# Performance work log

Measured on AMD Instinct MI355X. Metric: run time of the kernel, lower is better.

## Reference

```python
import jax, jax.numpy as jnp
import numpy as np
import math

D_MODEL = 512
DIM_K = 512
DIM_V = 512
N_HEADS = 8


def setup_inputs() -> dict:
    key = jax.random.key(0)
    ks = jax.random.split(key, 12)
    B, S = 2, 2048
    sc = 1.0 / math.sqrt(D_MODEL)
    return {
        "x": jax.random.normal(ks[0], (B, S, D_MODEL), dtype=jnp.float32),
        "y": jax.random.normal(ks[1], (B, S, D_MODEL), dtype=jnp.float32),
        # weights stored [in, out] so linear is x @ W + b
        "Wq": jax.random.normal(ks[2], (D_MODEL, DIM_K), dtype=jnp.float32) * sc,
        "bq": jnp.zeros((DIM_K,), dtype=jnp.float32),
        "Wk": jax.random.normal(ks[3], (D_MODEL, DIM_K), dtype=jnp.float32) * sc,
        "bk": jnp.zeros((DIM_K,), dtype=jnp.float32),
        "Wv": jax.random.normal(ks[4], (D_MODEL, DIM_V), dtype=jnp.float32) * sc,
        "bv": jnp.zeros((DIM_V,), dtype=jnp.float32),
        "Wo": jax.random.normal(ks[5], (DIM_V, D_MODEL), dtype=jnp.float32) * sc,
        "bo": jnp.zeros((D_MODEL,), dtype=jnp.float32),
    }


def reference(x, y, Wq, bq, Wk, bk, Wv, bv, Wo, bo):
    B, S, _ = x.shape
    H = N_HEADS
    Dh = DIM_K // H
    Dvh = DIM_V // H
    norm = 1.0 / math.sqrt(D_MODEL)  # note: original scales by 1/sqrt(d_model)

    # torch: q(x).reshape(-1, B, S, Dh) -> heads on leading dim (row-major)
    Q = (x @ Wq + bq).reshape(-1, B, S, Dh)      # [H,B,S,Dh]
    K = (y @ Wk + bk).reshape(-1, B, S, Dh)      # [H,B,S,Dh]
    V = (y @ Wv + bv).reshape(-1, B, S, Dvh)     # [H,B,S,Dvh]

    scores = jnp.einsum('hbqd,hbkd->hbqk', Q, K) * norm  # [H,B,S,S]

    # median-threshold mask: torch.median on even n returns lower middle value
    med_idx = (S - 1) // 2
    thre = jnp.sort(scores, axis=-1)[..., med_idx:med_idx + 1]  # [H,B,S,1]
    masked = scores - thre <= 0  # mask where score <= median
    scores = jnp.where(masked, -jnp.inf, scores)

    attn = jax.nn.softmax(scores, axis=-1)
    # dropout omitted (deterministic / eval mode)
    out = jnp.einsum('hbqk,hbkd->hbqd', attn, V)  # [H,B,S,Dvh]
    out = out.reshape(B, S, -1)                   # faithful row-major reshape
    return out @ Wo + bo
```

## Files before the change

### kernel.cpp

```cpp
#include <hip/hip_runtime.h>
#include <hip/hip_bf16.h>
#include <stdint.h>

#define SEQ    2048
#define DMODEL 512
#define NPANEL 16
#define NORM   0.044194173824159216f

typedef _Float16 f16;
typedef __attribute__((ext_vector_type(8))) _Float16 half8;
typedef __attribute__((ext_vector_type(2))) _Float16 half2v;
typedef __attribute__((ext_vector_type(4))) float f32x4;
typedef __attribute__((ext_vector_type(4))) unsigned int u32x4;

__device__ __forceinline__ unsigned umin2(unsigned a, unsigned b){ return a<b?a:b; }
__device__ __forceinline__ unsigned umax2(unsigned a, unsigned b){ return a>b?a:b; }

__global__ __launch_bounds__(256) void k_cvt(const float4* __restrict__ x,
                                             const float4* __restrict__ y,
                                             f16* __restrict__ xh, f16* __restrict__ xl,
                                             f16* __restrict__ yh, f16* __restrict__ yl){
  int i = blockIdx.x*256 + threadIdx.x;
  float4 a = x[i]; float4 b = y[i];
  half2v h0 = {(f16)a.x, (f16)a.y}, h1 = {(f16)a.z, (f16)a.w};
  *(half2v*)(xh + i*4)     = h0; *(half2v*)(xh + i*4 + 2) = h1;
  half2v l0 = {(f16)(a.x-(float)h0[0]), (f16)(a.y-(float)h0[1])};
  half2v l1 = {(f16)(a.z-(float)h1[0]), (f16)(a.w-(float)h1[1])};
  *(half2v*)(xl + i*4)     = l0; *(half2v*)(xl + i*4 + 2) = l1;
  half2v g0 = {(f16)b.x, (f16)b.y}, g1 = {(f16)b.z, (f16)b.w};
  *(half2v*)(yh + i*4)     = g0; *(half2v*)(yh + i*4 + 2) = g1;
  half2v m0 = {(f16)(b.x-(float)g0[0]), (f16)(b.y-(float)g0[1])};
  half2v m1 = {(f16)(b.z-(float)g1[0]), (f16)(b.w-(float)g1[1])};
  *(half2v*)(yl + i*4)     = m0; *(half2v*)(yl + i*4 + 2) = m1;
}

__global__ __launch_bounds__(256) void k_wt(const float* __restrict__ Wq, const float* __restrict__ Wk,
                                            const float* __restrict__ Wv, const float* __restrict__ Wo,
                                            f16* __restrict__ Wth, f16* __restrict__ Wtl){
  int z = blockIdx.z;
  const float* W = (z==0)?Wq:(z==1)?Wk:(z==2)?Wv:Wo;
  __shared__ float tile[64][65];
  int k0 = blockIdx.x*64, n0 = blockIdx.y*64;
  #pragma unroll
  for (int i = 0; i < 16; ++i){
    int s = threadIdx.x + i*256; int kl2 = s>>6, nl = s&63;
    tile[kl2][nl] = W[(k0+kl2)*512 + (n0+nl)];
  }
  __syncthreads();
  #pragma unroll
  for (int i = 0; i < 16; ++i){
    int s = threadIdx.x + i*256; int nl = s>>6, kl2 = s&63;
    float v = tile[kl2][nl];
    f16 h = (f16)v;
    int idx = z*262144 + (n0+nl)*512 + (k0+kl2);
    Wth[idx] = h;
    Wtl[idx] = (f16)(v - (float)h);
  }
}

template<int FINAL>
__global__ __launch_bounds__(256) void k_gemm(const f16* __restrict__ Ah0, const f16* __restrict__ Al0,
                                              const f16* __restrict__ Ah1, const f16* __restrict__ Al1,
                                              const f16* __restrict__ Wh, const f16* __restrict__ Wl,
                                              const float* __restrict__ b0, const float* __restrict__ b1,
                                              const float* __restrict__ b2,
                                              f16* __restrict__ Oq, float* __restrict__ Of){
  int z = blockIdx.z;
  const f16* A  = (z==0) ? Ah0 : Ah1;
  const f16* Alp= (z==0) ? Al0 : Al1;
  const f16* Bh = Wh + z*262144;
  const f16* Bl = Wl + z*262144;
  const float* bias = (z==0)?b0:(z==1)?b1:b2;
  const bool split = (FINAL==0) && (z<2);
  int m0 = blockIdx.x*128, n0 = blockIdx.y*128;

  __shared__ f16 Ahs[128][40], Bhs[128][40], Als[128][40], Bls[128][40];

  int t = threadIdx.x, l = t&63, w = t>>6;
  int wr = w>>1, wc = w&1;
  int lr = l&15, lk = l>>4;

  f32x4 acc[4][4];
  #pragma unroll
  for (int i=0;i<4;++i)
    #pragma unroll
    for (int j=0;j<4;++j) acc[i][j] = (f32x4){0.f,0.f,0.f,0.f};

  for (int ks = 0; ks < 16; ++ks){
    int k0 = ks*32;
    #pragma unroll
    for (int i = 0; i < 2; ++i){
      int s = t + i*256; int r = s>>2, kc = s&3;
      *(u32x4*)(&Ahs[r][kc*8]) = *(const u32x4*)(A   + (m0+r)*512 + k0 + kc*8);
      *(u32x4*)(&Bhs[r][kc*8]) = *(const u32x4*)(Bh  + (n0+r)*512 + k0 + kc*8);
      if (split){
        *(u32x4*)(&Als[r][kc*8]) = *(const u32x4*)(Alp + (m0+r)*512 + k0 + kc*8);
        *(u32x4*)(&Bls[r][kc*8]) = *(const u32x4*)(Bl  + (n0+r)*512 + k0 + kc*8);
      }
    }
    __syncthreads();
    half8 ah[4], bh2[4], al2[4], bl2[4];
    #pragma unroll
    for (int tm = 0; tm < 4; ++tm) ah[tm]  = *(const half8*)(&Ahs[wr*64 + tm*16 + lr][lk*8]);
    #pragma unroll
    for (int tn = 0; tn < 4; ++tn) bh2[tn] = *(const half8*)(&Bhs[wc*64 + tn*16 + lr][lk*8]);
    if (split){
      #pragma unroll
      for (int tm = 0; tm < 4; ++tm) al2[tm] = *(const half8*)(&Als[wr*64 + tm*16 + lr][lk*8]);
      #pragma unroll
      for (int tn = 0; tn < 4; ++tn) bl2[tn] = *(const half8*)(&Bls[wc*64 + tn*16 + lr][lk*8]);
    }
    #pragma unroll
    for (int tm = 0; tm < 4; ++tm)
      #pragma unroll
      for (int tn = 0; tn < 4; ++tn){
        acc[tm][tn] = __builtin_amdgcn_mfma_f32_16x16x32_f16(ah[tm], bh2[tn], acc[tm][tn], 0,0,0);
        if (split){
          acc[tm][tn] = __builtin_amdgcn_mfma_f32_16x16x32_f16(ah[tm], bl2[tn], acc[tm][tn], 0,0,0);
          acc[tm][tn] = __builtin_amdgcn_mfma_f32_16x16x32_f16(al2[tm], bh2[tn], acc[tm][tn], 0,0,0);
        }
      }
    __syncthreads();
  }

  #pragma unroll
  for (int tn = 0; tn < 4; ++tn){
    int n_g = n0 + wc*64 + tn*16 + lr;
    float bv = bias[n_g];
    #pragma unroll
    for (int tm = 0; tm < 4; ++tm){
      #pragma unroll
      for (int r = 0; r < 4; ++r){
        int m_g = m0 + wr*64 + tm*16 + lk*4 + r;
        float v = acc[tm][tn][r] + bv;
        size_t idx = (size_t)m_g*512 + n_g;
        if (FINAL){
          Of[idx] = v;
        } else if (z < 2){
          f16 h = (f16)v;
          Oq[(size_t)z*4194304 + idx] = h;
          Oq[(size_t)z*4194304 + 2097152 + idx] = (f16)(v - (float)h);
        } else {
          Oq[(size_t)4*2097152 + idx] = (f16)v;
        }
      }
    }
  }
}

__global__ __launch_bounds__(256) void k_vt(const unsigned short* __restrict__ V, unsigned short* __restrict__ Vt){
  int p = blockIdx.y;
  int t = threadIdx.x;
  int d = t & 63, sc = t >> 6;
  int s0b = blockIdx.x*32 + sc*8;
  const unsigned short* Vp = V + p*131072;
  unsigned short* Vtp = Vt + p*131072;
  typedef __attribute__((ext_vector_type(8))) short short8;
  short8 vv;
  #pragma unroll
  for (int j = 0; j < 8; ++j) vv[j] = (short)Vp[(s0b + j)*64 + d];
  *(short8*)(Vtp + d*2048 + s0b) = vv;
}

__global__ __launch_bounds__(512, 4) void k_attn(const f16* __restrict__ Qh, const f16* __restrict__ Ql,
                                                 const f16* __restrict__ Kh, const f16* __restrict__ Kl,
                                                 const f16* __restrict__ Vt, f16* __restrict__ O){
  extern __shared__ char scb[];
  __shared__ float rzs[16];
  __shared__ float red[1024];
  int p = blockIdx.x, qt = blockIdx.y;
  int s0 = qt*16;
  const f16* Qhp = Qh + p*131072;
  const f16* Qlp = Ql + p*131072;
  const f16* Khp = Kh + p*131072;
  const f16* Klp = Kl + p*131072;
  const f16* Vtp = Vt + p*131072;
  int t = threadIdx.x, l = t&63, w = t>>6;
  int lr = l&15, lk = l>>4;

  half8 qh[2], ql[2];
  #pragma unroll
  for (int f = 0; f < 2; ++f){
    qh[f] = *(const half8*)(Qhp + (s0+lr)*64 + f*32 + lk*8);
    ql[f] = *(const half8*)(Qlp + (s0+lr)*64 + f*32 + lk*8);
  }

  {
    const f16* Kbase = Khp + (w*128 + lr)*64 + lk*8;
    const f16* Lbase = Klp + (w*128 + lr)*64 + lk*8;
    #pragma unroll
    for (int bt = 0; bt < 2; ++bt){
      half8 kb0[4], kb1[4], lb0[4], lb1[4];
      #pragma unroll
      for (int i = 0; i < 4; ++i){
        const f16* ka = Kbase + (bt*4 + i)*1024;
        const f16* la = Lbase + (bt*4 + i)*1024;
        kb0[i] = *(const half8*)(ka);
        kb1[i] = *(const half8*)(ka + 32);
        lb0[i] = *(const half8*)(la);
        lb1[i] = *(const half8*)(la + 32);
      }
      #pragma unroll
      for (int i = 0; i < 4; ++i){
        f32x4 c1 = (f32x4){0.f,0.f,0.f,0.f};
        f32x4 c2 = (f32x4){0.f,0.f,0.f,0.f};
        f32x4 c3 = (f32x4){0.f,0.f,0.f,0.f};
        c1 = __builtin_amdgcn_mfma_f32_16x16x32_f16(qh[0], kb0[i], c1, 0,0,0);
        c2 = __builtin_amdgcn_mfma_f32_16x16x32_f16(qh[0], lb0[i], c2, 0,0,0);
        c3 = __builtin_amdgcn_mfma_f32_16x16x32_f16(ql[0], kb0[i], c3, 0,0,0);
        c1 = __builtin_amdgcn_mfma_f32_16x16x32_f16(qh[1], kb1[i], c1, 0,0,0);
        c2 = __builtin_amdgcn_mfma_f32_16x16x32_f16(qh[1], lb1[i], c2, 0,0,0);
        c3 = __builtin_amdgcn_mfma_f32_16x16x32_f16(ql[1], kb1[i], c3, 0,0,0);
        int n = w*128 + (bt*4 + i)*16 + lr;
        #pragma unroll
        for (int r = 0; r < 4; ++r){
          int row = lk*4 + r;
          *(float*)(scb + row*4096 + (((unsigned)(n*4)) ^ ((unsigned)(lk<<6)))) = c1[r] + c2[r] + c3[r];
        }
      }
    }
  }
  __syncthreads();

  unsigned ovA0[16], ovA1[16];
  {
    int row0 = w*2;
    unsigned C = ((unsigned)((row0>>2)&3))<<6;
    const char* rb0 = scb + row0*4096;
    const char* rb1 = rb0 + 4096;
    #pragma unroll
    for (int j = 0; j < 16; ++j){
      unsigned off = (((unsigned)((l + j*64)*4)) ^ C);
      unsigned u0 = *(const unsigned*)(rb0 + off);
      unsigned u1 = *(const unsigned*)(rb1 + off);
      ovA0[j] = ((int)u0 < 0) ? ~u0 : (u0 | 0x80000000u);
      ovA1[j] = ((int)u1 < 0) ? ~u1 : (u1 | 0x80000000u);
    }
  }
  __syncthreads();

  {
    const f16* Kbase = Khp + (1024 + w*128 + lr)*64 + lk*8;
    const f16* Lbase = Klp + (1024 + w*128 + lr)*64 + lk*8;
    #pragma unroll
    for (int bt = 0; bt < 4; ++bt){
      half8 kb0[2], kb1[2], lb0[2], lb1[2];
      #pragma unroll
      for (int i = 0; i < 2; ++i){
        const f16* ka = Kbase + (bt*2 + i)*1024;
        const f16* la = Lbase + (bt*2 + i)*1024;
        kb0[i] = *(const half8*)(ka);
        kb1[i] = *(const half8*)(ka + 32);
        lb0[i] = *(const half8*)(la);
        lb1[i] = *(const half8*)(la + 32);
      }
      #pragma unroll
      for (int i = 0; i < 2; ++i){
        f32x4 c1 = (f32x4){0.f,0.f,0.f,0.f};
        f32x4 c2 = (f32x4){0.f,0.f,0.f,0.f};
        f32x4 c3 = (f32x4){0.f,0.f,0.f,0.f};
        c1 = __builtin_amdgcn_mfma_f32_16x16x32_f16(qh[0], kb0[i], c1, 0,0,0);
        c2 = __builtin_amdgcn_mfma_f32_16x16x32_f16(qh[0], lb0[i], c2, 0,0,0);
        c3 = __builtin_amdgcn_mfma_f32_16x16x32_f16(ql[0], kb0[i], c3, 0,0,0);
        c1 = __builtin_amdgcn_mfma_f32_16x16x32_f16(qh[1], kb1[i], c1, 0,0,0);
        c2 = __builtin_amdgcn_mfma_f32_16x16x32_f16(qh[1], lb1[i], c2, 0,0,0);
        c3 = __builtin_amdgcn_mfma_f32_16x16x32_f16(ql[1], kb1[i], c3, 0,0,0);
        int n = w*128 + (bt*2 + i)*16 + lr;
        #pragma unroll
        for (int r = 0; r < 4; ++r){
          int row = lk*4 + r;
          *(float*)(scb + row*4096 + (((unsigned)(n*4)) ^ ((unsigned)(lk<<6)))) = c1[r] + c2[r] + c3[r];
        }
      }
    }
  }
  __syncthreads();

  #pragma unroll 1
  for (int rr = 0; rr < 2; ++rr){
    int row = w*2 + rr;
    const char* rb = scb + row*4096;
    unsigned C = ((unsigned)((row>>2)&3))<<6;
    unsigned o2[16];
    #pragma unroll
    for (int j = 0; j < 16; ++j){
      unsigned u = *(const unsigned*)(rb + (((unsigned)((l + j*64)*4)) ^ C));
      o2[j] = ((int)u < 0) ? ~u : (u | 0x80000000u);
    }
    unsigned umn = 0xFFFFFFFFu, umx = 0u;
    #pragma unroll
    for (int j = 0; j < 16; ++j){
      unsigned a = (rr==0) ? ovA0[j] : ovA1[j];
      umn = umin2(umn, umin2(a, o2[j]));
      umx = umax2(umax2(umx, a), o2[j]);
    }
    #pragma unroll
    for (int off2 = 1; off2 < 64; off2 <<= 1){
      umn = umin2(umn, (unsigned)__shfl_xor((int)umn, off2));
      umx = umax2(umx, (unsigned)__shfl_xor((int)umx, off2));
    }
    unsigned thr;
    {
      unsigned L = umn, R = umx;
      #pragma unroll 1
      for (;;){
        if (L >= R){ thr = R; break; }
        unsigned mid = L + ((R - L) >> 1);
        int c = 0;
        #pragma unroll
        for (int j = 0; j < 16; ++j){
          unsigned a = (rr==0) ? ovA0[j] : ovA1[j];
          c += (int)__popcll(__ballot(a <= mid));
          c += (int)__popcll(__ballot(o2[j] <= mid));
        }
        if (c == 1024){ thr = mid; break; }
        if (c > 1024) R = mid; else L = mid + 1;
      }
    }
    unsigned bmx = (umx & 0x80000000u) ? (umx & 0x7FFFFFFFu) : ~umx;
    float mx = __uint_as_float(bmx);
    float zs = 0.f;
    unsigned g = ((unsigned)(row & 7)) << 4;
    char* pb = scb + row*4096;
    #pragma unroll
    for (int j = 0; j < 32; ++j){
      unsigned a = (j < 16) ? ((rr==0) ? ovA0[j] : ovA1[j]) : o2[j-16];
      unsigned b = (a & 0x80000000u) ? (a & 0x7FFFFFFFu) : ~a;
      float v = __uint_as_float(b);
      float wgt = (a <= thr) ? 0.f : __expf((v - mx) * NORM);
      zs += wgt;
      unsigned col = (unsigned)((j & 15)*64 + l + (j >> 4)*1024);
      *(f16*)(pb + ((col*2) ^ g)) = (f16)wgt;
    }
    #pragma unroll
    for (int off2 = 1; off2 < 64; off2 <<= 1) zs += __shfl_xor(zs, off2);
    if (l == 0) rzs[row] = 1.f / zs;
  }
  __syncthreads();

  int oc = w & 3, kh2 = w >> 2;
  const f16* vbase = Vtp + (oc*16 + lr)*2048 + kh2*1024 + lk*8;
  const char* pbase = scb + lr*4096;
  unsigned pswz = ((unsigned)(lr & 7)) << 4;
  f32x4 o0 = (f32x4){0.f,0.f,0.f,0.f};
  f32x4 o1 = (f32x4){0.f,0.f,0.f,0.f};
  #pragma unroll
  for (int kb2 = 0; kb2 < 8; ++kb2){
    half8 pa[4], vb[4];
    #pragma unroll
    for (int i = 0; i < 4; ++i){
      int kc = kb2*4 + i;
      pa[i] = *(const half8*)(pbase + (((unsigned)((kh2*1024 + kc*32 + lk*8)*2)) ^ pswz));
      vb[i] = *(const half8*)(vbase + kc*32);
    }
    o0 = __builtin_amdgcn_mfma_f32_16x16x32_f16(pa[0], vb[0], o0, 0,0,0);
    o1 = __builtin_amdgcn_mfma_f32_16x16x32_f16(pa[1], vb[1], o1, 0,0,0);
    o0 = __builtin_amdgcn_mfma_f32_16x16x32_f16(pa[2], vb[2], o0, 0,0,0);
    o1 = __builtin_amdgcn_mfma_f32_16x16x32_f16(pa[3], vb[3], o1, 0,0,0);
  }
  f32x4 oa;
  #pragma unroll
  for (int r = 0; r < 4; ++r) oa[r] = o0[r] + o1[r];
  if (kh2 == 1){
    #pragma unroll
    for (int r = 0; r < 4; ++r) red[oc*256 + (lk*4+r)*16 + lr] = oa[r];
  }
  __syncthreads();
  if (kh2 == 0){
    #pragma unroll
    for (int r = 0; r < 4; ++r){
      int row = lk*4 + r;
      float v = (oa[r] + red[oc*256 + row*16 + lr]) * rzs[row];
      O[p*131072 + (s0+row)*64 + oc*16 + lr] = (f16)v;
    }
  }
}

extern "C" void kernel_launch(void* const* d_in, const int* in_sizes, int n_in,
                              void* d_out, int out_size, void* d_ws, size_t ws_size,
                              hipStream_t stream) {
  const float* x  = (const float*)d_in[0];
  const float* y  = (const float*)d_in[1];
  const float* Wq = (const float*)d_in[2];
  const float* bq = (const float*)d_in[3];
  const float* Wk = (const float*)d_in[4];
  const float* bk = (const float*)d_in[5];
  const float* Wv = (const float*)d_in[6];
  const float* bv = (const float*)d_in[7];
  const float* Wo = (const float*)d_in[8];
  const float* bo = (const float*)d_in[9];

  f16* ws = (f16*)d_ws;
  f16* xh  = ws;
  f16* xl  = ws + 2097152;
  f16* yh  = ws + 4194304;
  f16* yl  = ws + 6291456;
  f16* Wth = ws + 8388608;
  f16* Wtl = ws + 9437184;
  f16* QKV = ws + 10485760;
  f16* Vt  = ws;
  f16* Ob  = ws + 2097152;

  (void)hipFuncSetAttribute(reinterpret_cast<const void*>(k_attn),
                            hipFuncAttributeMaxDynamicSharedMemorySize, 65536);

  k_cvt<<<2048, 256, 0, stream>>>((const float4*)x, (const float4*)y, xh, xl, yh, yl);
  k_wt<<<dim3(8,8,4), 256, 0, stream>>>(Wq, Wk, Wv, Wo, Wth, Wtl);
  k_gemm<0><<<dim3(32,4,3), 256, 0, stream>>>(xh, xl, yh, yl, Wth, Wtl, bq, bk, bv, QKV, nullptr);
  k_vt<<<dim3(64,16), 256, 0, stream>>>((const unsigned short*)(QKV + 4*2097152), (unsigned short*)Vt);
  k_attn<<<dim3(16,128), 512, 65536, stream>>>(QKV, QKV + 2097152, QKV + 2*2097152, QKV + 3*2097152, Vt, Ob);
  k_gemm<1><<<dim3(32,4,1), 256, 0, stream>>>(Ob, Ob, Ob, Ob, Wth + 3*262144, Wtl, bo, bo, bo, nullptr, (float*)d_out);
}
```

Measured before the change: 290.6 us.

## Speed up median selection with interpolation search and DPP wave reductions

Rewrites the per-row median threshold search. It starts from the row mean as the first pivot and alternates interpolation steps (using the counts at the bracket ends) with bisection steps, so fewer counting iterations should be needed. Counting now sums per-lane comparisons followed by a single DPP/readlane wave sum, instead of one ballot and popcount per element. The min, max and exp-sum reductions also switch from shfl_xor to DPP row shifts plus readlane. This adds a float division per step and extra control flow, and the quality of the interpolation depends on how the scores are distributed.

Measured after the change: 302.2 us. +4.0%, slower.

```diff
diff --git a/kernel.cpp b/kernel.cpp
--- a/kernel.cpp
+++ b/kernel.cpp
@@ -15,6 +15,116 @@
 
 __device__ __forceinline__ unsigned umin2(unsigned a, unsigned b){ return a<b?a:b; }
 __device__ __forceinline__ unsigned umax2(unsigned a, unsigned b){ return a>b?a:b; }
+
+__device__ __forceinline__ int wsum_i(int v){
+  v += __builtin_amdgcn_update_dpp(0, v, 0x111, 0xf, 0xf, true);
+  v += __builtin_amdgcn_update_dpp(0, v, 0x112, 0xf, 0xf, true);
+  v += __builtin_amdgcn_update_dpp(0, v, 0x114, 0xf, 0xf, true);
+  v += __builtin_amdgcn_update_dpp(0, v, 0x118, 0xf, 0xf, true);
+  return __builtin_amdgcn_readlane(v,15) + __builtin_amdgcn_readlane(v,31)
+       + __builtin_amdgcn_readlane(v,47) + __builtin_amdgcn_readlane(v,63);
+}
+__device__ __forceinline__ float wsum_f(float v){
+  float t;
+  t = __int_as_float(__builtin_amdgcn_update_dpp(0, __float_as_int(v), 0x111, 0xf, 0xf, true)); v += t;
+  t = __int_as_float(__builtin_amdgcn_update_dpp(0, __float_as_int(v), 0x112, 0xf, 0xf, true)); v += t;
+  t = __int_as_float(__builtin_amdgcn_update_dpp(0, __float_as_int(v), 0x114, 0xf, 0xf, true)); v += t;
+  t = __int_as_float(__builtin_amdgcn_update_dpp(0, __float_as_int(v), 0x118, 0xf, 0xf, true)); v += t;
+  float r = __int_as_float(__builtin_amdgcn_readlane(__float_as_int(v),15));
+  r += __int_as_float(__builtin_amdgcn_readlane(__float_as_int(v),31));
+  r += __int_as_float(__builtin_amdgcn_readlane(__float_as_int(v),47));
+  r += __int_as_float(__builtin_amdgcn_readlane(__float_as_int(v),63));
+  return r;
+}
+__device__ __forceinline__ unsigned wmin_u(unsigned v){
+  unsigned t;
+  t = (unsigned)__builtin_amdgcn_update_dpp((int)v,(int)v,0x111,0xf,0xf,false); v = umin2(v,t);
+  t = (unsigned)__builtin_amdgcn_update_dpp((int)v,(int)v,0x112,0xf,0xf,false); v = umin2(v,t);
+  t = (unsigned)__builtin_amdgcn_update_dpp((int)v,(int)v,0x114,0xf,0xf,false); v = umin2(v,t);
+  t = (unsigned)__builtin_amdgcn_update_dpp((int)v,(int)v,0x118,0xf,0xf,false); v = umin2(v,t);
+  return umin2(umin2((unsigned)__builtin_amdgcn_readlane((int)v,15),(unsigned)__builtin_amdgcn_readlane((int)v,31)),
+               umin2((unsigned)__builtin_amdgcn_readlane((int)v,47),(unsigned)__builtin_amdgcn_readlane((int)v,63)));
+}
+__device__ __forceinline__ unsigned wmax_u(unsigned v){
+  unsigned t;
+  t = (unsigned)__builtin_amdgcn_update_dpp((int)v,(int)v,0x111,0xf,0xf,false); v = umax2(v,t);
+  t = (unsigned)__builtin_amdgcn_update_dpp((int)v,(int)v,0x112,0xf,0xf,false); v = umax2(v,t);
+  t = (unsigned)__builtin_amdgcn_update_dpp((int)v,(int)v,0x114,0xf,0xf,false); v = umax2(v,t);
+  t = (unsigned)__builtin_amdgcn_update_dpp((int)v,(int)v,0x118,0xf,0xf,false); v = umax2(v,t);
+  return umax2(umax2((unsigned)__builtin_amdgcn_readlane((int)v,15),(unsigned)__builtin_amdgcn_readlane((int)v,31)),
+               umax2((unsigned)__builtin_amdgcn_readlane((int)v,47),(unsigned)__builtin_amdgcn_readlane((int)v,63)));
+}
+
+__device__ __forceinline__ void sel_row(const unsigned (&a)[16], const unsigned (&b)[16],
+                                        char* pb, float* rzs, int row, int l){
+  unsigned vmn = 0xFFFFFFFFu, vmx = 0u;
+  float fs = 0.f;
+  #pragma unroll
+  for (int j = 0; j < 16; ++j){
+    vmn = umin2(vmn, umin2(a[j], b[j]));
+    vmx = umax2(umax2(vmx, a[j]), b[j]);
+    unsigned ba = (a[j] & 0x80000000u) ? (a[j] & 0x7FFFFFFFu) : ~a[j];
+    unsigned bb = (b[j] & 0x80000000u) ? (b[j] & 0x7FFFFFFFu) : ~b[j];
+    fs += __uint_as_float(ba) + __uint_as_float(bb);
+  }
+  unsigned umn = wmin_u(vmn);
+  unsigned umx = wmax_u(vmx);
+  float mu = wsum_f(fs) * (1.0f/2048.0f);
+  unsigned bmu = __float_as_uint(mu);
+  unsigned emu = ((int)bmu < 0) ? ~bmu : (bmu | 0x80000000u);
+
+  unsigned thr;
+  {
+    unsigned L = umn, R = umx, cL = 0, cR = 2048, mid = emu;
+    int it = 0;
+    #pragma unroll 1
+    for (;;){
+      if (L >= R){ thr = R; break; }
+      if (mid < L) mid = L;
+      if (mid > R - 1) mid = R - 1;
+      int c0=0,c1=0,c2=0,c3=0;
+      #pragma unroll
+      for (int j = 0; j < 4; ++j){
+        c0 += (a[j]    <= mid); c1 += (a[j+4]  <= mid);
+        c2 += (a[j+8]  <= mid); c3 += (a[j+12] <= mid);
+        c0 += (b[j]    <= mid); c1 += (b[j+4]  <= mid);
+        c2 += (b[j+8]  <= mid); c3 += (b[j+12] <= mid);
+      }
+      int c = wsum_i((c0+c1)+(c2+c3));
+      if (c == 1024){ thr = mid; break; }
+      if (c > 1024){ R = mid; cR = (unsigned)c; }
+      else         { L = mid + 1; cL = (unsigned)c; }
+      if (L >= R){ thr = R; break; }
+      unsigned span = R - L;
+      unsigned off;
+      if (it & 1) off = span >> 1;
+      else {
+        float f = (float)(1024 - (int)cL) * (float)span / (float)((int)cR - (int)cL);
+        off = (unsigned)(int)f;
+      }
+      if (off >= span) off = span - 1;
+      mid = L + off;
+      ++it;
+    }
+  }
+
+  unsigned bmx = (umx & 0x80000000u) ? (umx & 0x7FFFFFFFu) : ~umx;
+  float mx = __uint_as_float(bmx);
+  float zs = 0.f;
+  unsigned g = ((unsigned)(row & 7)) << 4;
+  #pragma unroll
+  for (int j = 0; j < 32; ++j){
+    unsigned vv = (j < 16) ? a[j] : b[j-16];
+    unsigned bb = (vv & 0x80000000u) ? (vv & 0x7FFFFFFFu) : ~vv;
+    float v = __uint_as_float(bb);
+    float wgt = (vv <= thr) ? 0.f : __expf((v - mx) * NORM);
+    zs += wgt;
+    unsigned col = (unsigned)((j & 15)*64 + l + (j >> 4)*1024);
+    *(f16*)(pb + ((col*2) ^ g)) = (f16)wgt;
+  }
+  float zt = wsum_f(zs);
+  if (l == 0) rzs[row] = 1.f / zt;
+}
 
 __global__ __launch_bounds__(256) void k_cvt(const float4* __restrict__ x,
                                              const float4* __restrict__ y,
@@ -276,65 +386,28 @@
   }
   __syncthreads();
 
-  #pragma unroll 1
-  for (int rr = 0; rr < 2; ++rr){
-    int row = w*2 + rr;
-    const char* rb = scb + row*4096;
-    unsigned C = ((unsigned)((row>>2)&3))<<6;
+  {
+    int row0 = w*2;
+    unsigned C = ((unsigned)((row0>>2)&3))<<6;
     unsigned o2[16];
-    #pragma unroll
-    for (int j = 0; j < 16; ++j){
-      unsigned u = *(const unsigned*)(rb + (((unsigned)((l + j*64)*4)) ^ C));
-      o2[j] = ((int)u < 0) ? ~u : (u | 0x80000000u);
-    }
-    unsigned umn = 0xFFFFFFFFu, umx = 0u;
-    #pragma unroll
-    for (int j = 0; j < 16; ++j){
-      unsigned a = (rr==0) ? ovA0[j] : ovA1[j];
-      umn = umin2(umn, umin2(a, o2[j]));
-      umx = umax2(umax2(umx, a), o2[j]);
-    }
-    #pragma unroll
-    for (int off2 = 1; off2 < 64; off2 <<= 1){
-      umn = umin2(umn, (unsigned)__shfl_xor((int)umn, off2));
-      umx = umax2(umx, (unsigned)__shfl_xor((int)umx, off2));
-    }
-    unsigned thr;
     {
-      unsigned L = umn, R = umx;
-      #pragma unroll 1
-      for (;;){
-        if (L >= R){ thr = R; break; }
-        unsigned mid = L + ((R - L) >> 1);
-        int c = 0;
-        #pragma unroll
-        for (int j = 0; j < 16; ++j){
-          unsigned a = (rr==0) ? ovA0[j] : ovA1[j];
-          c += (int)__popcll(__ballot(a <= mid));
-          c += (int)__popcll(__ballot(o2[j] <= mid));
-        }
-        if (c == 1024){ thr = mid; break; }
-        if (c > 1024) R = mid; else L = mid + 1;
-      }
-    }
-    unsigned bmx = (umx & 0x80000000u) ? (umx & 0x7FFFFFFFu) : ~umx;
-    float mx = __uint_as_float(bmx);
-    float zs = 0.f;
-    unsigned g = ((unsigned)(row & 7)) << 4;
-    char* pb = scb + row*4096;
-    #pragma unroll
-    for (int j = 0; j < 32; ++j){
-      unsigned a = (j < 16) ? ((rr==0) ? ovA0[j] : ovA1[j]) : o2[j-16];
-      unsigned b = (a & 0x80000000u) ? (a & 0x7FFFFFFFu) : ~a;
-      float v = __uint_as_float(b);
-      float wgt = (a <= thr) ? 0.f : __expf((v - mx) * NORM);
-      zs += wgt;
-      unsigned col = (unsigned)((j & 15)*64 + l + (j >> 4)*1024);
-      *(f16*)(pb + ((col*2) ^ g)) = (f16)wgt;
-    }
-    #pragma unroll
-    for (int off2 = 1; off2 < 64; off2 <<= 1) zs += __shfl_xor(zs, off2);
-    if (l == 0) rzs[row] = 1.f / zs;
+      const char* rb0 = scb + row0*4096;
+      #pragma unroll
+      for (int j = 0; j < 16; ++j){
+        unsigned u = *(const unsigned*)(rb0 + (((unsigned)((l + j*64)*4)) ^ C));
+        o2[j] = ((int)u < 0) ? ~u : (u | 0x80000000u);
+      }
+    }
+    sel_row(ovA0, o2, scb + row0*4096, rzs, row0, l);
+    {
+      const char* rb1 = scb + (row0+1)*4096;
+      #pragma unroll
+      for (int j = 0; j < 16; ++j){
+        unsigned u = *(const unsigned*)(rb1 + (((unsigned)((l + j*64)*4)) ^ C));
+        o2[j] = ((int)u < 0) ? ~u : (u | 0x80000000u);
+      }
+    }
+    sel_row(ovA1, o2, scb + (row0+1)*4096, rzs, row0+1, l);
   }
   __syncthreads();
 
```

## Process 32 query rows per attention block to reuse K and V loads

Applied to the files above, without the earlier changes.

The attention kernel now handles 32 query rows per block instead of 16, using 1024 threads and 128KB of dynamic LDS for the score rows. Each wave loads a K column tile once and runs MFMAs for two row tiles, so global K/V traffic per query row is roughly halved. The PV stage is split four ways along the key dimension, with a larger LDS reduction buffer to combine the partial sums. The cost is much higher LDS use per block (about 152KB), which likely allows only one block per CU and lowers occupancy and latency hiding.

New measurement: 308.8 us. 6.3% more time.

```diff
diff --git a/kernel.cpp b/kernel.cpp
--- a/kernel.cpp
+++ b/kernel.cpp
@@ -162,14 +162,14 @@
   *(short8*)(Vtp + d*2048 + s0b) = vv;
 }
 
-__global__ __launch_bounds__(512, 4) void k_attn(const f16* __restrict__ Qh, const f16* __restrict__ Ql,
-                                                 const f16* __restrict__ Kh, const f16* __restrict__ Kl,
-                                                 const f16* __restrict__ Vt, f16* __restrict__ O){
+__global__ __launch_bounds__(1024, 4) void k_attn(const f16* __restrict__ Qh, const f16* __restrict__ Ql,
+                                                  const f16* __restrict__ Kh, const f16* __restrict__ Kl,
+                                                  const f16* __restrict__ Vt, f16* __restrict__ O){
   extern __shared__ char scb[];
-  __shared__ float rzs[16];
-  __shared__ float red[1024];
+  __shared__ float rzs[32];
+  __shared__ float red[6144];
   int p = blockIdx.x, qt = blockIdx.y;
-  int s0 = qt*16;
+  int s0 = qt*32;
   const f16* Qhp = Qh + p*131072;
   const f16* Qlp = Ql + p*131072;
   const f16* Khp = Kh + p*131072;
@@ -178,43 +178,43 @@
   int t = threadIdx.x, l = t&63, w = t>>6;
   int lr = l&15, lk = l>>4;
 
-  half8 qh[2], ql[2];
-  #pragma unroll
-  for (int f = 0; f < 2; ++f){
-    qh[f] = *(const half8*)(Qhp + (s0+lr)*64 + f*32 + lk*8);
-    ql[f] = *(const half8*)(Qlp + (s0+lr)*64 + f*32 + lk*8);
-  }
+  half8 qh[2][2], qlo[2][2];
+  #pragma unroll
+  for (int rt = 0; rt < 2; ++rt)
+    #pragma unroll
+    for (int f = 0; f < 2; ++f){
+      qh[rt][f]  = *(const half8*)(Qhp + (s0 + rt*16 + lr)*64 + f*32 + lk*8);
+      qlo[rt][f] = *(const half8*)(Qlp + (s0 + rt*16 + lr)*64 + f*32 + lk*8);
+    }
+
+  unsigned ovA0[16], ovA1[16];
 
   {
-    const f16* Kbase = Khp + (w*128 + lr)*64 + lk*8;
-    const f16* Lbase = Klp + (w*128 + lr)*64 + lk*8;
-    #pragma unroll
-    for (int bt = 0; bt < 2; ++bt){
-      half8 kb0[4], kb1[4], lb0[4], lb1[4];
-      #pragma unroll
-      for (int i = 0; i < 4; ++i){
-        const f16* ka = Kbase + (bt*4 + i)*1024;
-        const f16* la = Lbase + (bt*4 + i)*1024;
-        kb0[i] = *(const half8*)(ka);
-        kb1[i] = *(const half8*)(ka + 32);
-        lb0[i] = *(const half8*)(la);
-        lb1[i] = *(const half8*)(la + 32);
-      }
-      #pragma unroll
-      for (int i = 0; i < 4; ++i){
+    const f16* Kb = Khp + (w*64 + lr)*64 + lk*8;
+    const f16* Lb = Klp + (w*64 + lr)*64 + lk*8;
+    #pragma unroll
+    for (int ct = 0; ct < 4; ++ct){
+      const f16* ka = Kb + ct*1024;
+      const f16* la = Lb + ct*1024;
+      half8 kb0 = *(const half8*)(ka);
+      half8 kb1 = *(const half8*)(ka + 32);
+      half8 lb0 = *(const half8*)(la);
+      half8 lb1 = *(const half8*)(la + 32);
+      #pragma unroll
+      for (int rt = 0; rt < 2; ++rt){
         f32x4 c1 = (f32x4){0.f,0.f,0.f,0.f};
         f32x4 c2 = (f32x4){0.f,0.f,0.f,0.f};
         f32x4 c3 = (f32x4){0.f,0.f,0.f,0.f};
-        c1 = __builtin_amdgcn_mfma_f32_16x16x32_f16(qh[0], kb0[i], c1, 0,0,0);
-        c2 = __builtin_amdgcn_mfma_f32_16x16x32_f16(qh[0], lb0[i], c2, 0,0,0);
-        c3 = __builtin_amdgcn_mfma_f32_16x16x32_f16(ql[0], kb0[i], c3, 0,0,0);
-        c1 = __builtin_amdgcn_mfma_f32_16x16x32_f16(qh[1], kb1[i], c1, 0,0,0);
-        c2 = __builtin_amdgcn_mfma_f32_16x16x32_f16(qh[1], lb1[i], c2, 0,0,0);
-        c3 = __builtin_amdgcn_mfma_f32_16x16x32_f16(ql[1], kb1[i], c3, 0,0,0);
-        int n = w*128 + (bt*4 + i)*16 + lr;
+        c1 = __builtin_amdgcn_mfma_f32_16x16x32_f16(qh[rt][0],  kb0, c1, 0,0,0);
+        c2 = __builtin_amdgcn_mfma_f32_16x16x32_f16(qh[rt][0],  lb0, c2, 0,0,0);
+        c3 = __builtin_amdgcn_mfma_f32_16x16x32_f16(qlo[rt][0], kb0, c3, 0,0,0);
+        c1 = __builtin_amdgcn_mfma_f32_16x16x32_f16(qh[rt][1],  kb1, c1, 0,0,0);
+        c2 = __builtin_amdgcn_mfma_f32_16x16x32_f16(qh[rt][1],  lb1, c2, 0,0,0);
+        c3 = __builtin_amdgcn_mfma_f32_16x16x32_f16(qlo[rt][1], kb1, c3, 0,0,0);
+        int n = w*64 + ct*16 + lr;
         #pragma unroll
         for (int r = 0; r < 4; ++r){
-          int row = lk*4 + r;
+          int row = rt*16 + lk*4 + r;
           *(float*)(scb + row*4096 + (((unsigned)(n*4)) ^ ((unsigned)(lk<<6)))) = c1[r] + c2[r] + c3[r];
         }
       }
@@ -222,12 +222,10 @@
   }
   __syncthreads();
 
-  unsigned ovA0[16], ovA1[16];
   {
-    int row0 = w*2;
-    unsigned C = ((unsigned)((row0>>2)&3))<<6;
-    const char* rb0 = scb + row0*4096;
-    const char* rb1 = rb0 + 4096;
+    unsigned C = ((unsigned)((w>>2)&3))<<6;
+    const char* rb0 = scb + w*4096;
+    const char* rb1 = scb + (w+16)*4096;
     #pragma unroll
     for (int j = 0; j < 16; ++j){
       unsigned off = (((unsigned)((l + j*64)*4)) ^ C);
@@ -240,35 +238,31 @@
   __syncthreads();
 
   {
-    const f16* Kbase = Khp + (1024 + w*128 + lr)*64 + lk*8;
-    const f16* Lbase = Klp + (1024 + w*128 + lr)*64 + lk*8;
-    #pragma unroll
-    for (int bt = 0; bt < 4; ++bt){
-      half8 kb0[2], kb1[2], lb0[2], lb1[2];
-      #pragma unroll
-      for (int i = 0; i < 2; ++i){
-        const f16* ka = Kbase + (bt*2 + i)*1024;
-        const f16* la = Lbase + (bt*2 + i)*1024;
-        kb0[i] = *(const half8*)(ka);
-        kb1[i] = *(const half8*)(ka + 32);
-        lb0[i] = *(const half8*)(la);
-        lb1[i] = *(const half8*)(la + 32);
-      }
-      #pragma unroll
-      for (int i = 0; i < 2; ++i){
+    const f16* Kb = Khp + (1024 + w*64 + lr)*64 + lk*8;
+    const f16* Lb = Klp + (1024 + w*64 + lr)*64 + lk*8;
+    #pragma unroll
+    for (int ct = 0; ct < 4; ++ct){
+      const f16* ka = Kb + ct*1024;
+      const f16* la = Lb + ct*1024;
+      half8 kb0 = *(const half8*)(ka);
+      half8 kb1 = *(const half8*)(ka + 32);
+      half8 lb0 = *(const half8*)(la);
+      half8 lb1 = *(const half8*)(la + 32);
+      #pragma unroll
+      for (int rt = 0; rt < 2; ++rt){
         f32x4 c1 = (f32x4){0.f,0.f,0.f,0.f};
         f32x4 c2 = (f32x4){0.f,0.f,0.f,0.f};
         f32x4 c3 = (f32x4){0.f,0.f,0.f,0.f};
-        c1 = __builtin_amdgcn_mfma_f32_16x16x32_f16(qh[0], kb0[i], c1, 0,0,0);
-        c2 = __builtin_amdgcn_mfma_f32_16x16x32_f16(qh[0], lb0[i], c2, 0,0,0);
-        c3 = __builtin_amdgcn_mfma_f32_16x16x32_f16(ql[0], kb0[i], c3, 0,0,0);
-        c1 = __builtin_amdgcn_mfma_f32_16x16x32_f16(qh[1], kb1[i], c1, 0,0,0);
-        c2 = __builtin_amdgcn_mfma_f32_16x16x32_f16(qh[1], lb1[i], c2, 0,0,0);
-        c3 = __builtin_amdgcn_mfma_f32_16x16x32_f16(ql[1], kb1[i], c3, 0,0,0);
-        int n = w*128 + (bt*2 + i)*16 + lr;
+        c1 = __builtin_amdgcn_mfma_f32_16x16x32_f16(qh[rt][0],  kb0, c1, 0,0,0);
+        c2 = __builtin_amdgcn_mfma_f32_16x16x32_f16(qh[rt][0],  lb0, c2, 0,0,0);
+        c3 = __builtin_amdgcn_mfma_f32_16x16x32_f16(qlo[rt][0], kb0, c3, 0,0,0);
+        c1 = __builtin_amdgcn_mfma_f32_16x16x32_f16(qh[rt][1],  kb1, c1, 0,0,0);
+        c2 = __builtin_amdgcn_mfma_f32_16x16x32_f16(qh[rt][1],  lb1, c2, 0,0,0);
+        c3 = __builtin_amdgcn_mfma_f32_16x16x32_f16(qlo[rt][1], kb1, c3, 0,0,0);
+        int n = w*64 + ct*16 + lr;
         #pragma unroll
         for (int r = 0; r < 4; ++r){
-          int row = lk*4 + r;
+          int row = rt*16 + lk*4 + r;
           *(float*)(scb + row*4096 + (((unsigned)(n*4)) ^ ((unsigned)(lk<<6)))) = c1[r] + c2[r] + c3[r];
         }
       }
@@ -278,9 +272,9 @@
 
   #pragma unroll 1
   for (int rr = 0; rr < 2; ++rr){
-    int row = w*2 + rr;
+    int row = w + rr*16;
     const char* rb = scb + row*4096;
-    unsigned C = ((unsigned)((row>>2)&3))<<6;
+    unsigned C = ((unsigned)((w>>2)&3))<<6;
     unsigned o2[16];
     #pragma unroll
     for (int j = 0; j < 16; ++j){
@@ -338,41 +332,48 @@
   }
   __syncthreads();
 
-  int oc = w & 3, kh2 = w >> 2;
-  const f16* vbase = Vtp + (oc*16 + lr)*2048 + kh2*1024 + lk*8;
-  const char* pbase = scb + lr*4096;
+  int oc = w & 3, q = w >> 2;
+  const f16* vbase = Vtp + (oc*16 + lr)*2048 + q*512 + lk*8;
   unsigned pswz = ((unsigned)(lr & 7)) << 4;
-  f32x4 o0 = (f32x4){0.f,0.f,0.f,0.f};
-  f32x4 o1 = (f32x4){0.f,0.f,0.f,0.f};
-  #pragma unroll
-  for (int kb2 = 0; kb2 < 8; ++kb2){
-    half8 pa[4], vb[4];
-    #pragma unroll
-    for (int i = 0; i < 4; ++i){
-      int kc = kb2*4 + i;
-      pa[i] = *(const half8*)(pbase + (((unsigned)((kh2*1024 + kc*32 + lk*8)*2)) ^ pswz));
-      vb[i] = *(const half8*)(vbase + kc*32);
-    }
-    o0 = __builtin_amdgcn_mfma_f32_16x16x32_f16(pa[0], vb[0], o0, 0,0,0);
-    o1 = __builtin_amdgcn_mfma_f32_16x16x32_f16(pa[1], vb[1], o1, 0,0,0);
-    o0 = __builtin_amdgcn_mfma_f32_16x16x32_f16(pa[2], vb[2], o0, 0,0,0);
-    o1 = __builtin_amdgcn_mfma_f32_16x16x32_f16(pa[3], vb[3], o1, 0,0,0);
-  }
-  f32x4 oa;
-  #pragma unroll
-  for (int r = 0; r < 4; ++r) oa[r] = o0[r] + o1[r];
-  if (kh2 == 1){
-    #pragma unroll
-    for (int r = 0; r < 4; ++r) red[oc*256 + (lk*4+r)*16 + lr] = oa[r];
-  }
-  __syncthreads();
-  if (kh2 == 0){
-    #pragma unroll
-    for (int r = 0; r < 4; ++r){
-      int row = lk*4 + r;
-      float v = (oa[r] + red[oc*256 + row*16 + lr]) * rzs[row];
-      O[p*131072 + (s0+row)*64 + oc*16 + lr] = (f16)v;
-    }
+  f32x4 a00 = (f32x4){0.f,0.f,0.f,0.f};
+  f32x4 a01 = (f32x4){0.f,0.f,0.f,0.f};
+  f32x4 a10 = (f32x4){0.f,0.f,0.f,0.f};
+  f32x4 a11 = (f32x4){0.f,0.f,0.f,0.f};
+  #pragma unroll 4
+  for (int kc = 0; kc < 16; ++kc){
+    half8 vb = *(const half8*)(vbase + kc*32);
+    unsigned poff = (((unsigned)((q*512 + kc*32 + lk*8)*2)) ^ pswz);
+    half8 pa0 = *(const half8*)(scb + lr*4096 + poff);
+    half8 pa1 = *(const half8*)(scb + (16 + lr)*4096 + poff);
+    if (kc & 1){
+      a01 = __builtin_amdgcn_mfma_f32_16x16x32_f16(pa0, vb, a01, 0,0,0);
+      a11 = __builtin_amdgcn_mfma_f32_16x16x32_f16(pa1, vb, a11, 0,0,0);
+    } else {
+      a00 = __builtin_amdgcn_mfma_f32_16x16x32_f16(pa0, vb, a00, 0,0,0);
+      a10 = __builtin_amdgcn_mfma_f32_16x16x32_f16(pa1, vb, a10, 0,0,0);
+    }
+  }
+  f32x4 oa[2];
+  #pragma unroll
+  for (int r = 0; r < 4; ++r){ oa[0][r] = a00[r] + a01[r]; oa[1][r] = a10[r] + a11[r]; }
+  if (q > 0){
+    #pragma unroll
+    for (int rt = 0; rt < 2; ++rt)
+      #pragma unroll
+      for (int r = 0; r < 4; ++r)
+        red[(q-1)*2048 + rt*1024 + (lk*4+r)*64 + oc*16 + lr] = oa[rt][r];
+  }
+  __syncthreads();
+  if (q == 0){
+    #pragma unroll
+    for (int rt = 0; rt < 2; ++rt)
+      #pragma unroll
+      for (int r = 0; r < 4; ++r){
+        int row = rt*16 + lk*4 + r;
+        int ci = rt*1024 + (lk*4+r)*64 + oc*16 + lr;
+        float v = (oa[rt][r] + red[ci] + red[2048 + ci] + red[4096 + ci]) * rzs[row];
+        O[p*131072 + (s0+row)*64 + oc*16 + lr] = (f16)v;
+      }
   }
 }
 
@@ -402,12 +403,12 @@
   f16* Ob  = ws + 2097152;
 
   (void)hipFuncSetAttribute(reinterpret_cast<const void*>(k_attn),
-                            hipFuncAttributeMaxDynamicSharedMemorySize, 65536);
+                            hipFuncAttributeMaxDynamicSharedMemorySize, 131072);
 
   k_cvt<<<2048, 256, 0, stream>>>((const float4*)x, (const float4*)y, xh, xl, yh, yl);
   k_wt<<<dim3(8,8,4), 256, 0, stream>>>(Wq, Wk, Wv, Wo, Wth, Wtl);
   k_gemm<0><<<dim3(32,4,3), 256, 0, stream>>>(xh, xl, yh, yl, Wth, Wtl, bq, bk, bv, QKV, nullptr);
   k_vt<<<dim3(64,16), 256, 0, stream>>>((const unsigned short*)(QKV + 4*2097152), (unsigned short*)Vt);
-  k_attn<<<dim3(16,128), 512, 65536, stream>>>(QKV, QKV + 2097152, QKV + 2*2097152, QKV + 3*2097152, Vt, Ob);
+  k_attn<<<dim3(16,64), 1024, 131072, stream>>>(QKV, QKV + 2097152, QKV + 2*2097152, QKV + 3*2097152, Vt, Ob);
   k_gemm<1><<<dim3(32,4,1), 256, 0, stream>>>(Ob, Ob, Ob, Ob, Wth + 3*262144, Wtl, bo, bo, bo, nullptr, (float*)d_out);
 }
```
